# Optimization experiments

Hardware: AMD Instinct MI355X
Metric: run time of the kernel (lower is better)

Reference implementation:

```python
import jax, jax.numpy as jnp
import numpy as np

IN_DIM = 512
HEADS = 8
HEAD_DIM = IN_DIM // HEADS
SCALE = HEAD_DIM ** -0.5


def setup_inputs() -> dict:
    key = jax.random.key(0)
    ks = jax.random.split(key, 9)
    B, C, H, W = 16, IN_DIM, 32, 32
    std = 1.0 / np.sqrt(C)  # ~ conv2d default init scale
    inp = {
        "x": jax.random.normal(ks[0], (B, C, H, W), dtype=jnp.float32),
        "wq": jax.random.normal(ks[1], (C, C), dtype=jnp.float32) * std,
        "bq": jax.random.normal(ks[2], (C,), dtype=jnp.float32) * std,
        "wk": jax.random.normal(ks[3], (C, C), dtype=jnp.float32) * std,
        "bk": jax.random.normal(ks[4], (C,), dtype=jnp.float32) * std,
        "wv": jax.random.normal(ks[5], (C, C), dtype=jnp.float32) * std,
        "bv": jax.random.normal(ks[6], (C,), dtype=jnp.float32) * std,
        "wo": jax.random.normal(ks[7], (C, C), dtype=jnp.float32) * std,
        "bo": jax.random.normal(ks[8], (C,), dtype=jnp.float32) * std,
        "gamma": jnp.zeros((1,), dtype=jnp.float32) + 0.1,  # learned residual scale
    }
    return inp


def reference(x, wq, bq, wk, bk, wv, bv, wo, bo, gamma):
    B, C, H, W = x.shape
    N = H * W
    hd = HEAD_DIM
    # flatten spatial: [B, C, N]
    xf = x.reshape(B, C, N)
    # 1x1 convs == channel matmuls: [B, C, N]
    q = jnp.einsum('oc,bcn->bon', wq, xf) + bq[None, :, None]
    k = jnp.einsum('oc,bcn->bon', wk, xf) + bk[None, :, None]
    v = jnp.einsum('oc,bcn->bon', wv, xf) + bv[None, :, None]
    # split heads: [B, heads, head_dim, N]
    q = q.reshape(B, HEADS, hd, N)
    k = k.reshape(B, HEADS, hd, N)
    v = v.reshape(B, HEADS, hd, N)
    # energy[b,h,i,j] = sum_d q[b,h,d,i] * k[b,h,d,j]
    energy = jnp.einsum('bhdi,bhdj->bhij', q, k) * SCALE
    attn = jax.nn.softmax(energy, axis=-1)  # [B, heads, N, N]
    # out[b,h,d,i] = sum_j attn[b,h,i,j] * v[b,h,d,j]
    out = jnp.einsum('bhij,bhdj->bhdi', attn, v)
    out = out.reshape(B, C, N)
    out = jnp.einsum('oc,bcn->bon', wo, out) + bo[None, :, None]
    y = gamma[0] * out.reshape(B, C, H, W) + x
    return y
```

## Files before the change

kernel.cpp:

```cpp
#include <hip/hip_runtime.h>
#include <hip/hip_bf16.h>

#define BB 16
#define CC 512
#define HH 8
#define DD 64
#define NN 1024

using f32x4  = __attribute__((ext_vector_type(4))) float;
typedef __bf16 bf16x8 __attribute__((ext_vector_type(8)));
typedef __bf16 bf16x4 __attribute__((ext_vector_type(4)));

#define MFMA16(a, b, c) __builtin_amdgcn_mfma_f32_16x16x32_bf16((a), (b), (c), 0, 0, 0)

#define WAITVM12 asm volatile("s_waitcnt vmcnt(12)" ::: "memory")
#define WAITVM8  asm volatile("s_waitcnt vmcnt(8)" ::: "memory")
#define WAITVM6  asm volatile("s_waitcnt vmcnt(6)" ::: "memory")
#define WAITVM4  asm volatile("s_waitcnt vmcnt(4)" ::: "memory")
#define WAITVM0  asm volatile("s_waitcnt vmcnt(0)" ::: "memory")
#define BARRIER __builtin_amdgcn_s_barrier()
#define SCHEDB  __builtin_amdgcn_sched_barrier(0)

__device__ __forceinline__ void glds16(const __hip_bfloat16* g, __hip_bfloat16* l) {
  typedef __attribute__((address_space(1))) const void gv_t;
  typedef __attribute__((address_space(3))) void lv_t;
  __builtin_amdgcn_global_load_lds((gv_t*)g, (lv_t*)l, 16, 0, 0);
}

__global__ __launch_bounds__(256) void k_prep(
    const float* __restrict__ x, __hip_bfloat16* __restrict__ xT,
    __hip_bfloat16* __restrict__ xbf,
    const float* __restrict__ wq, const float* __restrict__ wk,
    const float* __restrict__ wv, const float* __restrict__ wo,
    __hip_bfloat16* __restrict__ wqb) {
  __shared__ float tile[64][65];
  const int L = blockIdx.x;
  const int t = threadIdx.x;
  if (L >= 2048) {
    const int j = L - 2048;
    const int mat = j >> 8;
    const float* s = (mat == 0) ? wq : (mat == 1) ? wk : (mat == 2) ? wv : wo;
    __hip_bfloat16* o = wqb + (size_t)mat * CC * CC;
    const int i = ((j & 255) * 256 + t) * 4;
    float4 v = *(const float4*)(s + i);
    alignas(8) __hip_bfloat16 tm[4];
    tm[0] = __float2bfloat16(v.x);
    tm[1] = __float2bfloat16(v.y);
    tm[2] = __float2bfloat16(v.z);
    tm[3] = __float2bfloat16(v.w);
    *(bf16x4*)(o + i) = *(const bf16x4*)tm;
    return;
  }
  const int c = L & 7, r = L >> 3;
  const int b  = c * 2 + (r >> 7);
  const int rr = r & 127;
  const int bn = (rr & 15) * 64;
  const int bc = (rr >> 4) * 64;

  const float* xb = x + ((size_t)b * CC + bc) * NN + bn;
  __hip_bfloat16* xbo = xbf + ((size_t)b * CC + bc) * NN + bn;
  const int r0 = t >> 4;
  const int c0 = (t & 15) * 4;
  for (int p = 0; p < 4; ++p) {
    const int rw = r0 + p * 16;
    float4 v = *(const float4*)(xb + (size_t)rw * NN + c0);
    tile[rw][c0 + 0] = v.x;
    tile[rw][c0 + 1] = v.y;
    tile[rw][c0 + 2] = v.z;
    tile[rw][c0 + 3] = v.w;
    alignas(8) __hip_bfloat16 tm[4];
    tm[0] = __float2bfloat16(v.x);
    tm[1] = __float2bfloat16(v.y);
    tm[2] = __float2bfloat16(v.z);
    tm[3] = __float2bfloat16(v.w);
    *(bf16x4*)(xbo + (size_t)rw * NN + c0) = *(const bf16x4*)tm;
  }
  __syncthreads();

  __hip_bfloat16* xo = xT + ((size_t)b * NN + bn) * CC + bc;
  const int rn0 = t >> 3;
  const int cc0 = (t & 7) * 8;
  for (int p = 0; p < 2; ++p) {
    const int rn = rn0 + p * 32;
    alignas(16) __hip_bfloat16 tmp[8];
    for (int j = 0; j < 8; ++j) tmp[j] = __float2bfloat16(tile[cc0 + j][rn]);
    *(bf16x8*)(xo + (size_t)rn * CC + cc0) = *(const bf16x8*)tmp;
  }
}

__global__ __launch_bounds__(512, 2) void k_gemm_qkv(
    const __hip_bfloat16* __restrict__ Wqkv,
    const __hip_bfloat16* __restrict__ Xt,
    const float* __restrict__ bq, const float* __restrict__ bk,
    const float* __restrict__ bv,
    __hip_bfloat16* __restrict__ qT, __hip_bfloat16* __restrict__ kT,
    __hip_bfloat16* __restrict__ vO, float qscale) {
  __shared__ __hip_bfloat16 Wl[3][8192];
  __shared__ __hip_bfloat16 Xl[3][16384];
  const int ot = blockIdx.y * 128;
  const int ng = blockIdx.x * 256;
  const int sector = blockIdx.y >> 2;
  const int t = threadIdx.x;
  const int w = t >> 6, l = t & 63;
  const int wr = w >> 2, wc = w & 3;
  const int lg = l >> 4, lr16 = l & 15;

  f32x4 acc[4][4] = {};

  const __hip_bfloat16* Wp = Wqkv + (size_t)ot * CC;
  const __hip_bfloat16* Xp = Xt + (size_t)ng * CC;
  const int srow = w * 8 + (l >> 3);
  const int scol = ((l & 7) ^ ((l >> 3) & 7)) * 8;
  const __hip_bfloat16* asrc = Wp + (size_t)srow * CC + scol;
  const __hip_bfloat16* bsrc = Xp + (size_t)srow * CC + scol;

  auto STAGE = [&](int buf, int kt) {
#pragma unroll
    for (int i = 0; i < 2; ++i)
      glds16(asrc + (size_t)(i * 64) * CC + kt * 64, &Wl[buf][(w * 8 + i * 64) * 64]);
#pragma unroll
    for (int i = 0; i < 4; ++i)
      glds16(bsrc + (size_t)(i * 64) * CC + kt * 64, &Xl[buf][(w * 8 + i * 64) * 64]);
  };

  const int s7 = lr16 & 7;
  const int slot0 = (lg ^ s7) * 8;
  const int slot1 = ((4 + lg) ^ s7) * 8;
  const int rowA = (wr * 64 + lr16) * 64;
  const int rowB = (wc * 64 + lr16) * 64;

  auto STEP = [&](int bn) {
    const __hip_bfloat16* Wb = &Wl[bn][0];
    const __hip_bfloat16* Xb = &Xl[bn][0];
#pragma unroll
    for (int ks = 0; ks < 2; ++ks) {
      const int sl = ks ? slot1 : slot0;
      bf16x8 af[4], bfr[4];
#pragma unroll
      for (int mi = 0; mi < 4; ++mi) af[mi] = *(const bf16x8*)(Wb + rowA + mi * 1024 + sl);
#pragma unroll
      for (int nj = 0; nj < 4; ++nj) bfr[nj] = *(const bf16x8*)(Xb + rowB + nj * 1024 + sl);
      __builtin_amdgcn_s_setprio(1);
#pragma unroll
      for (int mi = 0; mi < 4; ++mi)
#pragma unroll
        for (int nj = 0; nj < 4; ++nj)
          acc[mi][nj] = MFMA16(af[mi], bfr[nj], acc[mi][nj]);
      __builtin_amdgcn_s_setprio(0);
    }
  };

  STAGE(0, 0);
  STAGE(1, 1);
  STAGE(2, 2);
  for (int kt = 0; kt < 8; ++kt) {
    if (kt < 6) { WAITVM12; } else if (kt == 6) { WAITVM6; } else { WAITVM0; }
    BARRIER; SCHEDB;
    STEP(kt % 3);
    BARRIER;
    if (kt < 5) STAGE(kt % 3, kt + 3);
  }

  const float* bias = (sector == 0) ? bq : (sector == 1) ? bk : bv;
  const float scale = (sector == 0) ? qscale : 1.0f;
  __hip_bfloat16* outT = (sector == 0) ? qT : kT;
  const int bb = ng >> 10;
  const int nb = ng & 1023;

#pragma unroll
  for (int mi = 0; mi < 4; ++mi) {
    const int og = ot + wr * 64 + mi * 16 + lg * 4;
    const int o0 = og & 511;
#pragma unroll
    for (int nj = 0; nj < 4; ++nj) {
      const int n = nb + wc * 64 + nj * 16 + lr16;
      if (sector < 2) {
        alignas(8) __hip_bfloat16 tmp[4];
#pragma unroll
        for (int rj = 0; rj < 4; ++rj)
          tmp[rj] = __float2bfloat16((acc[mi][nj][rj] + bias[o0 + rj]) * scale);
        const int hh = o0 >> 6, d0 = o0 & 63;
        *(bf16x4*)(outT + (((size_t)(bb * HH + hh)) * NN + n) * DD + d0) =
            *(const bf16x4*)tmp;
      } else {
#pragma unroll
        for (int rj = 0; rj < 4; ++rj)
          vO[((size_t)bb * CC + o0 + rj) * NN + n] =
              __float2bfloat16(acc[mi][nj][rj] + bias[o0 + rj]);
      }
    }
  }
}

__global__ __launch_bounds__(256, 4) void k_gemm_o(
    const __hip_bfloat16* __restrict__ W,
    const __hip_bfloat16* __restrict__ Xt,
    const float* __restrict__ bias,
    const __hip_bfloat16* __restrict__ xbf,
    const float* __restrict__ gamma,
    float* __restrict__ y) {
  __shared__ __hip_bfloat16 Wl[2][4096];
  __shared__ __hip_bfloat16 Xl[2][4096];
  const int b  = blockIdx.z;
  const int ot = blockIdx.y * 128;
  const int nt = blockIdx.x * 128;
  const int t  = threadIdx.x;
  const int w  = t >> 6, l = t & 63;
  const int wr = w >> 1, wc = w & 1;
  const int lg = l >> 4, lr16 = l & 15;

  f32x4 acc[4][4] = {};

  const int srow = w * 16 + (l >> 2);
  const int scol = ((l & 3) ^ ((l >> 3) & 3)) * 8;
  const __hip_bfloat16* ws0 = W + (size_t)(ot + srow) * CC + scol;
  const __hip_bfloat16* xs0 = Xt + ((size_t)b * NN + nt + srow) * CC + scol;

  const int sx  = (lg ^ ((lr16 >> 1) & 3)) * 8;
  const int rdA = (wr * 64 + lr16) * 32 + sx;
  const int rdB = (wc * 64 + lr16) * 32 + sx;

#define STAGEO(bn, k0)                                        \
  do {                                                        \
    glds16(ws0 + (k0), &Wl[bn][w * 512]);                     \
    glds16(ws0 + (size_t)64 * CC + (k0), &Wl[bn][2048 + w * 512]); \
    glds16(xs0 + (k0), &Xl[bn][w * 512]);                     \
    glds16(xs0 + (size_t)64 * CC + (k0), &Xl[bn][2048 + w * 512]); \
  } while (0)

  STAGEO(0, 0);
  for (int kt = 0; kt < 16; ++kt) {
    WAITVM0;
    BARRIER; SCHEDB;
    if (kt < 15) STAGEO((kt + 1) & 1, (kt + 1) * 32);
    const __hip_bfloat16* Wb = &Wl[kt & 1][0];
    const __hip_bfloat16* Xb = &Xl[kt & 1][0];
    bf16x8 af[4], bfr[4];
#pragma unroll
    for (int mi = 0; mi < 4; ++mi) af[mi] = *(const bf16x8*)(Wb + rdA + mi * 512);
#pragma unroll
    for (int nj = 0; nj < 4; ++nj) bfr[nj] = *(const bf16x8*)(Xb + rdB + nj * 512);
    __builtin_amdgcn_s_setprio(1);
#pragma unroll
    for (int mi = 0; mi < 4; ++mi)
#pragma unroll
      for (int nj = 0; nj < 4; ++nj)
        acc[mi][nj] = MFMA16(af[mi], bfr[nj], acc[mi][nj]);
    __builtin_amdgcn_s_setprio(0);
  }
#undef STAGEO

  const float g = gamma[0];
  for (int mi = 0; mi < 4; ++mi) {
    const int o0 = ot + wr * 64 + mi * 16 + lg * 4;
    for (int nj = 0; nj < 4; ++nj) {
      const int n = nt + wc * 64 + nj * 16 + lr16;
      for (int rj = 0; rj < 4; ++rj) {
        const size_t idx = ((size_t)b * CC + o0 + rj) * NN + n;
        y[idx] = g * (acc[mi][nj][rj] + bias[o0 + rj]) + __bfloat162float(xbf[idx]);
      }
    }
  }
}

__global__ __launch_bounds__(256, 2) void k_attn(
    const __hip_bfloat16* __restrict__ qT,
    const __hip_bfloat16* __restrict__ kT,
    const __hip_bfloat16* __restrict__ v,
    __hip_bfloat16* __restrict__ attT) {
  __shared__ __hip_bfloat16 Kl[3][4096];
  __shared__ __hip_bfloat16 Vl[3][4096];

  const int L = blockIdx.x;
  const int c = L & 7, s = L >> 3;
  const int bh = c * 16 + (s >> 2);
  const int i0 = (s & 3) * 256;
  const int b = bh >> 3, h = bh & 7;
  const int t  = threadIdx.x;
  const int w  = t >> 6, l = t & 63;
  const int lg = l >> 4, lr = l & 15;

  const __hip_bfloat16* qb = qT + ((size_t)(b * HH + h)) * NN * DD;
  const __hip_bfloat16* kb = kT + ((size_t)(b * HH + h)) * NN * DD;
  const __hip_bfloat16* vb = v + ((size_t)b * CC + h * DD) * NN;

  bf16x8 qf[4][2];
#pragma unroll
  for (int g = 0; g < 4; ++g) {
    const __hip_bfloat16* qp = qb + (size_t)(i0 + w * 64 + g * 16 + lr) * DD + lg * 8;
    qf[g][0] = *(const bf16x8*)qp;
    qf[g][1] = *(const bf16x8*)(qp + 32);
  }

  const int rA = w * 8 + (l >> 3);
  const int rB = rA + 32;
  const int sA = (l & 7) ^ ((rA & 3) ^ (((rA >> 3) & 1) << 2));
  const __hip_bfloat16* gKA = kb + rA * DD + sA * 8;
  const __hip_bfloat16* gKB = kb + rB * DD + sA * 8;
  const __hip_bfloat16* gVA = vb + (size_t)rA * NN + sA * 8;
  const __hip_bfloat16* gVB = vb + (size_t)rB * NN + sA * 8;

  auto STAGE = [&](int bufn, int tile) {
    glds16(gKA + (size_t)tile * 4096, &Kl[bufn][w * 512]);
    glds16(gKB + (size_t)tile * 4096, &Kl[bufn][2048 + w * 512]);
    glds16(gVA + tile * 64, &Vl[bufn][w * 512]);
    glds16(gVB + tile * 64, &Vl[bufn][2048 + w * 512]);
  };

  const int swzK = (lr & 3) ^ (((lr >> 2) & 1) << 2);
  const int krl  = 8 * (lr >> 2) + (lr & 3);
  const int offK0 = krl * 64 + ((lg ^ swzK) * 8);
  const int offK1 = krl * 64 + (((lg + 4) ^ swzK) * 8);
  const int swzV = (lr & 3) ^ (((lr >> 3) & 1) << 2);

  f32x4 accO[4][4] = {};
  f32x4 accL[4] = {};
  const bf16x8 ones = {(__bf16)1.f, (__bf16)1.f, (__bf16)1.f, (__bf16)1.f,
                       (__bf16)1.f, (__bf16)1.f, (__bf16)1.f, (__bf16)1.f};

  STAGE(0, 0);
  STAGE(1, 1);
  STAGE(2, 2);

  for (int tile = 0; tile < 16; ++tile) {
    const int bufn = tile % 3;
    if (tile < 14) { WAITVM8; } else if (tile == 14) { WAITVM4; } else { WAITVM0; }
    BARRIER; SCHEDB;

    const __hip_bfloat16* Kb = &Kl[bufn][0];
    const __hip_bfloat16* Vb = &Vl[bufn][0];

    __builtin_amdgcn_s_setprio(1);
    f32x4 st[4][4];
#pragma unroll
    for (int jt = 0; jt < 4; ++jt) {
      const int jo = (jt >> 1) * 2048 + (jt & 1) * 256;
      bf16x8 kf0 = *(const bf16x8*)(Kb + jo + offK0);
      bf16x8 kf1 = *(const bf16x8*)(Kb + jo + offK1);
#pragma unroll
      for (int g = 0; g < 4; ++g) {
        f32x4 a = {};
        a = MFMA16(kf0, qf[g][0], a);
        a = MFMA16(kf1, qf[g][1], a);
        st[g][jt] = a;
      }
    }
    __builtin_amdgcn_s_setprio(0);

    bf16x8 pf[4][2];
#pragma unroll
    for (int g = 0; g < 4; ++g) {
      union { bf16x8 v8; __hip_bfloat16 h[8]; } pk0, pk1;
#pragma unroll
      for (int jt = 0; jt < 4; ++jt)
#pragma unroll
        for (int rj = 0; rj < 4; ++rj) {
          const float p = __builtin_amdgcn_exp2f(st[g][jt][rj]);
          if (jt < 2) pk0.h[(jt & 1) * 4 + rj] = __float2bfloat16(p);
          else        pk1.h[(jt & 1) * 4 + rj] = __float2bfloat16(p);
        }
      pf[g][0] = pk0.v8;
      pf[g][1] = pk1.v8;
    }

    __builtin_amdgcn_s_setprio(1);
#pragma unroll
    for (int ks = 0; ks < 2; ++ks) {
#pragma unroll
      for (int dt = 0; dt < 4; ++dt) {
        bf16x8 vf = *(const bf16x8*)(Vb + (dt * 16 + lr) * 64 + (((ks * 4 + lg) ^ swzV) * 8));
#pragma unroll
        for (int g = 0; g < 4; ++g)
          accO[g][dt] = MFMA16(pf[g][ks], vf, accO[g][dt]);
      }
#pragma unroll
      for (int g = 0; g < 4; ++g)
        accL[g] = MFMA16(pf[g][ks], ones, accL[g]);
    }
    __builtin_amdgcn_s_setprio(0);

    BARRIER;
    if (tile < 13) STAGE(bufn, tile + 3);
  }

#pragma unroll
  for (int g = 0; g < 4; ++g)
#pragma unroll
    for (int dt = 0; dt < 4; ++dt) {
      f32x4 o;
#pragma unroll
      for (int rj = 0; rj < 4; ++rj) o[rj] = accO[g][dt][rj] / accL[g][rj];
#pragma unroll
      for (int rj = 0; rj < 4; ++rj) {
        const int i = i0 + w * 64 + g * 16 + 4 * lg + rj;
        const int d = dt * 16 + lr;
        attT[((size_t)b * NN + i) * CC + h * DD + d] = __float2bfloat16(o[rj]);
      }
    }
}

extern "C" void kernel_launch(void* const* d_in, const int* in_sizes, int n_in,
                              void* d_out, int out_size, void* d_ws, size_t ws_size,
                              hipStream_t stream) {
  const float* x     = (const float*)d_in[0];
  const float* wq    = (const float*)d_in[1];
  const float* bq    = (const float*)d_in[2];
  const float* wk    = (const float*)d_in[3];
  const float* bk    = (const float*)d_in[4];
  const float* wv    = (const float*)d_in[5];
  const float* bv    = (const float*)d_in[6];
  const float* wo    = (const float*)d_in[7];
  const float* bo    = (const float*)d_in[8];
  const float* gamma = (const float*)d_in[9];
  float* y = (float*)d_out;

  char* ws = (char*)d_ws;
  const size_t szT = (size_t)BB * NN * CC * 2;
  __hip_bfloat16* xT  = (__hip_bfloat16*)(ws);
  __hip_bfloat16* qT  = (__hip_bfloat16*)(ws + szT);
  __hip_bfloat16* kTb = (__hip_bfloat16*)(ws + 2 * szT);
  __hip_bfloat16* vB  = (__hip_bfloat16*)(ws + 3 * szT);
  __hip_bfloat16* xbf = (__hip_bfloat16*)(ws + 4 * szT);
  __hip_bfloat16* wqb = (__hip_bfloat16*)(ws + 5 * szT);
  __hip_bfloat16* wob = wqb + (size_t)3 * CC * CC;

  k_prep<<<dim3(2048 + 1024), 256, 0, stream>>>(x, xT, xbf, wq, wk, wv, wo, wqb);

  const float qsc = 0.125f * 1.44269504f;
  k_gemm_qkv<<<dim3(16384 / 256, 1536 / 128, 1), 512, 0, stream>>>(
      wqb, xT, bq, bk, bv, qT, kTb, vB, qsc);

  k_attn<<<dim3(BB * HH * (NN / 256)), 256, 0, stream>>>(qT, kTb, vB, xT);

  k_gemm_o<<<dim3(NN / 128, CC / 128, BB), 256, 0, stream>>>(
      wob, xT, bo, xbf, gamma, y);
}
```

Before: 117.7 us.

## Split QKV GEMM K-step into two half-phases with interleaved A/B staging

Restructures the QKV projection GEMM main loop so each K tile runs in two MFMA phases over the A rows. B fragments are cached in registers across both phases, and the global-to-LDS loads for the weight (A) and activation (B) tiles are issued separately at different points in the loop. The aim is to overlap LDS reads and global prefetch with MFMA work in a ping-pong style, keeping the matrix units busier. In exchange it adds more barriers per iteration, carefully tuned vmcnt wait counts that must match the load order, and higher register pressure.

Measured after the change: 119.9 us. Within noise of the previous version (+1.9%).

```diff
diff --git a/kernel.cpp b/kernel.cpp
--- a/kernel.cpp
+++ b/kernel.cpp
@@ -13,7 +13,7 @@
 
 #define MFMA16(a, b, c) __builtin_amdgcn_mfma_f32_16x16x32_bf16((a), (b), (c), 0, 0, 0)
 
-#define WAITVM12 asm volatile("s_waitcnt vmcnt(12)" ::: "memory")
+#define WAITVM10 asm volatile("s_waitcnt vmcnt(10)" ::: "memory")
 #define WAITVM8  asm volatile("s_waitcnt vmcnt(8)" ::: "memory")
 #define WAITVM6  asm volatile("s_waitcnt vmcnt(6)" ::: "memory")
 #define WAITVM4  asm volatile("s_waitcnt vmcnt(4)" ::: "memory")
@@ -106,6 +106,7 @@
   const int lg = l >> 4, lr16 = l & 15;
 
   f32x4 acc[4][4] = {};
+  bf16x8 bfr[4][2];
 
   const __hip_bfloat16* Wp = Wqkv + (size_t)ot * CC;
   const __hip_bfloat16* Xp = Xt + (size_t)ng * CC;
@@ -114,10 +115,12 @@
   const __hip_bfloat16* asrc = Wp + (size_t)srow * CC + scol;
   const __hip_bfloat16* bsrc = Xp + (size_t)srow * CC + scol;
 
-  auto STAGE = [&](int buf, int kt) {
+  auto SA = [&](int buf, int kt) {
 #pragma unroll
     for (int i = 0; i < 2; ++i)
       glds16(asrc + (size_t)(i * 64) * CC + kt * 64, &Wl[buf][(w * 8 + i * 64) * 64]);
+  };
+  auto SB = [&](int buf, int kt) {
 #pragma unroll
     for (int i = 0; i < 4; ++i)
       glds16(bsrc + (size_t)(i * 64) * CC + kt * 64, &Xl[buf][(w * 8 + i * 64) * 64]);
@@ -129,36 +132,60 @@
   const int rowA = (wr * 64 + lr16) * 64;
   const int rowB = (wc * 64 + lr16) * 64;
 
-  auto STEP = [&](int bn) {
-    const __hip_bfloat16* Wb = &Wl[bn][0];
-    const __hip_bfloat16* Xb = &Xl[bn][0];
-#pragma unroll
-    for (int ks = 0; ks < 2; ++ks) {
-      const int sl = ks ? slot1 : slot0;
-      bf16x8 af[4], bfr[4];
-#pragma unroll
-      for (int mi = 0; mi < 4; ++mi) af[mi] = *(const bf16x8*)(Wb + rowA + mi * 1024 + sl);
-#pragma unroll
-      for (int nj = 0; nj < 4; ++nj) bfr[nj] = *(const bf16x8*)(Xb + rowB + nj * 1024 + sl);
-      __builtin_amdgcn_s_setprio(1);
-#pragma unroll
-      for (int mi = 0; mi < 4; ++mi)
-#pragma unroll
-        for (int nj = 0; nj < 4; ++nj)
-          acc[mi][nj] = MFMA16(af[mi], bfr[nj], acc[mi][nj]);
-      __builtin_amdgcn_s_setprio(0);
-    }
-  };
-
-  STAGE(0, 0);
-  STAGE(1, 1);
-  STAGE(2, 2);
-  for (int kt = 0; kt < 8; ++kt) {
-    if (kt < 6) { WAITVM12; } else if (kt == 6) { WAITVM6; } else { WAITVM0; }
-    BARRIER; SCHEDB;
-    STEP(kt % 3);
+  SA(0, 0); SA(1, 1); SB(0, 0); SB(1, 1); SB(2, 2);
+  WAITVM8;
+  BARRIER;
+
+  for (int j = 0; j < 8; ++j) {
+    const int bn = j % 3;
+    const __hip_bfloat16* Ab = &Wl[bn][0];
+    const __hip_bfloat16* Bb = &Xl[bn][0];
+
+    bf16x8 a0 = *(const bf16x8*)(Ab + rowA + 0 * 1024 + slot0);
+    bf16x8 a1 = *(const bf16x8*)(Ab + rowA + 0 * 1024 + slot1);
+    bf16x8 a2 = *(const bf16x8*)(Ab + rowA + 1 * 1024 + slot0);
+    bf16x8 a3 = *(const bf16x8*)(Ab + rowA + 1 * 1024 + slot1);
+#pragma unroll
+    for (int nj = 0; nj < 4; ++nj) {
+      bfr[nj][0] = *(const bf16x8*)(Bb + rowB + nj * 1024 + slot0);
+      bfr[nj][1] = *(const bf16x8*)(Bb + rowB + nj * 1024 + slot1);
+    }
+    if (j < 6) SA((j + 2) % 3, j + 2);
     BARRIER;
-    if (kt < 5) STAGE(kt % 3, kt + 3);
+    asm volatile("s_waitcnt lgkmcnt(0)" ::: "memory");
+    SCHEDB;
+    __builtin_amdgcn_s_setprio(1);
+#pragma unroll
+    for (int nj = 0; nj < 4; ++nj) {
+      acc[0][nj] = MFMA16(a0, bfr[nj][0], acc[0][nj]);
+      acc[0][nj] = MFMA16(a1, bfr[nj][1], acc[0][nj]);
+      acc[1][nj] = MFMA16(a2, bfr[nj][0], acc[1][nj]);
+      acc[1][nj] = MFMA16(a3, bfr[nj][1], acc[1][nj]);
+    }
+    __builtin_amdgcn_s_setprio(0);
+    BARRIER;
+
+    a0 = *(const bf16x8*)(Ab + rowA + 2 * 1024 + slot0);
+    a1 = *(const bf16x8*)(Ab + rowA + 2 * 1024 + slot1);
+    a2 = *(const bf16x8*)(Ab + rowA + 3 * 1024 + slot0);
+    a3 = *(const bf16x8*)(Ab + rowA + 3 * 1024 + slot1);
+    if (j < 5) SB(bn, j + 3);
+    if (j < 5)      { WAITVM10; }
+    else if (j == 5) { WAITVM6; }
+    else if (j == 6) { WAITVM0; }
+    BARRIER;
+    asm volatile("s_waitcnt lgkmcnt(0)" ::: "memory");
+    SCHEDB;
+    __builtin_amdgcn_s_setprio(1);
+#pragma unroll
+    for (int nj = 0; nj < 4; ++nj) {
+      acc[2][nj] = MFMA16(a0, bfr[nj][0], acc[2][nj]);
+      acc[2][nj] = MFMA16(a1, bfr[nj][1], acc[2][nj]);
+      acc[3][nj] = MFMA16(a2, bfr[nj][0], acc[3][nj]);
+      acc[3][nj] = MFMA16(a3, bfr[nj][1], acc[3][nj]);
+    }
+    __builtin_amdgcn_s_setprio(0);
+    BARRIER;
   }
 
   const float* bias = (sector == 0) ? bq : (sector == 1) ? bk : bv;
```
